# Performance work log

Hardware: AMD Instinct MI355X
Metric: run time of the kernel (lower is better)

Reference implementation:

```python
import jax, jax.numpy as jnp
import numpy as np

D_IN = 1024
D_OUT = 1024
N_HEADS = 16
D_H = D_OUT // N_HEADS


def setup_inputs() -> dict:
    key = jax.random.key(0)
    k_x, k_q, k_k, k_v = jax.random.split(key, 4)
    x = jax.random.normal(k_x, (4, 2048, D_IN), dtype=jnp.float32)
    s = 1.0 / np.sqrt(D_IN)
    # weights stored as [d_in, d_out] (transpose of torch Linear.weight)
    W_q = jax.random.uniform(k_q, (D_IN, D_OUT), dtype=jnp.float32, minval=-s, maxval=s)
    W_k = jax.random.uniform(k_k, (D_IN, D_OUT), dtype=jnp.float32, minval=-s, maxval=s)
    W_v = jax.random.uniform(k_v, (D_IN, D_OUT), dtype=jnp.float32, minval=-s, maxval=s)
    return {"x": x, "W_q": W_q, "W_k": W_k, "W_v": W_v}


def reference(x, W_q, W_k, W_v):
    B, T, _ = x.shape
    # QKV projections -> [B, H, T, d_h]
    def split_heads(y):
        return y.reshape(B, T, N_HEADS, D_H).transpose(0, 2, 1, 3)
    q = split_heads(x @ W_q)
    k = split_heads(x @ W_k)
    v = split_heads(x @ W_v)
    # attention scores [B, H, T, T]
    scores = jnp.einsum('bhqd,bhkd->bhqk', q, k)
    causal = jnp.tril(jnp.ones((T, T), dtype=bool))  # True = keep
    scores = jnp.where(causal, scores, -jnp.inf)
    weights = jax.nn.softmax(scores / np.sqrt(D_H), axis=-1)
    ctx = jnp.einsum('bhqk,bhkd->bhqd', weights, v)  # [B,H,T,d_h]
    return ctx.transpose(0, 2, 1, 3).reshape(B, T, D_OUT)
```

## Files before the change

### kernel.cpp

```cpp
#include <hip/hip_runtime.h>
#include <stdint.h>

typedef float f32x4 __attribute__((ext_vector_type(4)));
typedef __bf16 bf16x8 __attribute__((ext_vector_type(8)));

#define LOG2E 1.4426950408889634f
#define SCL2 (0.125f * LOG2E)

static __device__ __forceinline__ unsigned short f2bf(float f) {
  unsigned int u = __builtin_bit_cast(unsigned int, f);
  u += 0x7fffu + ((u >> 16) & 1u);
  return (unsigned short)(u >> 16);
}

static __device__ __forceinline__ void gload16(const void* g, void* l) {
  __builtin_amdgcn_global_load_lds(
      (const __attribute__((address_space(1))) unsigned int*)g,
      (__attribute__((address_space(3))) unsigned int*)l, 16, 0, 0);
}

__global__ void cvt_x_kernel(const float* __restrict__ x, unsigned short* __restrict__ xb) {
  size_t i = ((size_t)blockIdx.x * 256 + threadIdx.x) * 8;
  const float4 a = *(const float4*)(x + i);
  const float4 b = *(const float4*)(x + i + 4);
  union { unsigned short us[8]; uint4 u; } o;
  o.us[0] = f2bf(a.x); o.us[1] = f2bf(a.y); o.us[2] = f2bf(a.z); o.us[3] = f2bf(a.w);
  o.us[4] = f2bf(b.x); o.us[5] = f2bf(b.y); o.us[6] = f2bf(b.z); o.us[7] = f2bf(b.w);
  *(uint4*)(xb + i) = o.u;
}

__global__ void wt_kernel(const float* __restrict__ Wq, const float* __restrict__ Wk,
                          const float* __restrict__ Wv, unsigned short* __restrict__ Wt) {
  __shared__ float t[32][33];
  const int z = blockIdx.z;
  const float* W = (z == 0) ? Wq : ((z == 1) ? Wk : Wv);
  unsigned short* o = Wt + (size_t)z * 1048576;
  const int k0 = blockIdx.y * 32, n0 = blockIdx.x * 32;
  const int tx = threadIdx.x, ty = threadIdx.y;
#pragma unroll
  for (int i = 0; i < 4; ++i)
    t[ty + i * 8][tx] = W[(size_t)(k0 + ty + i * 8) * 1024 + n0 + tx];
  __syncthreads();
#pragma unroll
  for (int i = 0; i < 4; ++i)
    o[(size_t)(n0 + ty + i * 8) * 1024 + k0 + tx] = f2bf(t[tx][ty + i * 8]);
}

__global__ __launch_bounds__(256) void gemm_qkv(
    const unsigned short* __restrict__ xb, const unsigned short* __restrict__ Wt,
    unsigned short* __restrict__ Qb, unsigned short* __restrict__ Kb,
    unsigned short* __restrict__ Vtb) {
  __shared__ uint4 ldsab[2048];
  char* ldsc = (char*)ldsab;
  const int tid = threadIdx.x;
  const int lane = tid & 63;
  const int li = lane & 15, g = lane >> 4;
  const int wv = tid >> 6, wr = wv >> 1, wc = wv & 1;
  const int z = blockIdx.z;
  const int m0 = blockIdx.y * 128, n0 = blockIdx.x * 128;
  const char* Abase = (const char*)xb;
  const char* Bbase = (const char*)(Wt + (size_t)z * 1048576);

  const f32x4 fz = {0.f, 0.f, 0.f, 0.f};
  f32x4 acc[4][4];
#pragma unroll
  for (int m = 0; m < 4; ++m)
#pragma unroll
    for (int n = 0; n < 4; ++n) acc[m][n] = fz;

  for (int kt = 0; kt < 16; ++kt) {
    __syncthreads();
#pragma unroll
    for (int i = 0; i < 4; ++i) {
      const int c = i * 256 + tid, r = c >> 3, cr = c & 7;
      gload16(Abase + (size_t)(m0 + r) * 2048 + kt * 128 + ((cr ^ (r & 7)) * 16),
              ldsc + c * 16);
      gload16(Bbase + (size_t)(n0 + r) * 2048 + kt * 128 + ((cr ^ (r & 7)) * 16),
              ldsc + 16384 + c * 16);
    }
    __syncthreads();
#pragma unroll
    for (int ks = 0; ks < 2; ++ks) {
      bf16x8 a[4], b[4];
#pragma unroll
      for (int m = 0; m < 4; ++m) {
        const int ra = wr * 64 + m * 16 + li;
        a[m] = *(const bf16x8*)(ldsc + ra * 128 + (((ks * 4 + g) ^ (ra & 7)) * 16));
      }
#pragma unroll
      for (int n = 0; n < 4; ++n) {
        const int rb = wc * 64 + n * 16 + li;
        b[n] = *(const bf16x8*)(ldsc + 16384 + rb * 128 + (((ks * 4 + g) ^ (rb & 7)) * 16));
      }
#pragma unroll
      for (int m = 0; m < 4; ++m)
#pragma unroll
        for (int n = 0; n < 4; ++n)
          acc[m][n] = __builtin_amdgcn_mfma_f32_16x16x32_bf16(a[m], b[n], acc[m][n], 0, 0, 0);
    }
  }

  unsigned short* dst = (z == 0) ? Qb : ((z == 1) ? Kb : Vtb);
  const float sc = (z == 0) ? SCL2 : 1.0f;
#pragma unroll
  for (int m = 0; m < 4; ++m) {
#pragma unroll
    for (int r = 0; r < 4; ++r) {
      const int mg = m0 + wr * 64 + m * 16 + g * 4 + r;
      const int bI = mg >> 11, t = mg & 2047;
#pragma unroll
      for (int n = 0; n < 4; ++n) {
        const int ng = n0 + wc * 64 + n * 16 + li;
        const int h = ng >> 6, d = ng & 63;
        const unsigned short v = f2bf(acc[m][n][r] * sc);
        if (z == 2)
          dst[((size_t)(bI * 16 + h) * 64 + d) * 2048 + t] = v;
        else
          dst[((size_t)(bI * 16 + h) * 2048 + t) * 64 + d] = v;
      }
    }
  }
}

__global__ __launch_bounds__(512, 4) void attn_kernel(
    const unsigned short* __restrict__ Qb, const unsigned short* __restrict__ Kb,
    const unsigned short* __restrict__ Vtb, float* __restrict__ out) {
  __shared__ uint4 lds[4096];
  char* ldsc = (char*)lds;
  const int L = blockIdx.x;
  const int W = (L & 7) * 64 + (L >> 3);
  const int bh = W >> 3;
  const int qp = W & 7;
  const int tid = threadIdx.x;
  const int lane = tid & 63, wv = tid >> 6;
  const int grp = wv >> 2, wq = wv & 3;
  const int t256 = tid & 255;
  const int li = lane & 15, g = lane >> 4;

  char* gbase = ldsc + grp * 32768;

  const char* Qrow = (const char*)Qb + (size_t)bh * 2048 * 128;
  const char* Krow = (const char*)Kb + (size_t)bh * 2048 * 128;
  const char* Vrow = (const char*)Vtb + (size_t)bh * 64 * 4096;
  const int bI = bh >> 4, h = bh & 15;
  const f32x4 fz = {0.f, 0.f, 0.f, 0.f};

  union { unsigned int u[4]; bf16x8 v; } onesu;
  onesu.u[0] = 0x3F803F80u; onesu.u[1] = 0x3F803F80u;
  onesu.u[2] = 0x3F803F80u; onesu.u[3] = 0x3F803F80u;
  const bf16x8 ones = onesu.v;

  auto stage = [&](int b, int kt) {
#pragma unroll
    for (int i = 0; i < 2; ++i) {
      const int c = i * 256 + t256, r = c >> 3, cr = c & 7;
      gload16(Krow + (size_t)(kt * 64 + r) * 128 + ((cr ^ (r & 7)) * 16),
              gbase + b * 16384 + c * 16);
      gload16(Vrow + (size_t)r * 4096 + kt * 128 + ((cr ^ (r & 7)) * 16),
              gbase + b * 16384 + 8192 + c * 16);
    }
  };

  for (int half = 0; half < 2; ++half) {
    const int qt = half ? (15 - qp) : qp;
    const int q0 = qt * 128;
    const int qw = q0 + wq * 32;
    const int hc = qt + 1;
    const int kbeg = grp ? hc : 0;

    uint4 qf[2][2];
#pragma unroll
    for (int nq = 0; nq < 2; ++nq)
#pragma unroll
      for (int ks = 0; ks < 2; ++ks)
        qf[nq][ks] = *(const uint4*)(Qrow + (size_t)(qw + nq * 16 + li) * 128 + ks * 64 + g * 16);

    float mrow[2] = {-1e30f, -1e30f};
    float lrow[2] = {0.0f, 0.0f};
    f32x4 lsum[2] = {fz, fz};
    f32x4 ctx[4][2];
#pragma unroll
    for (int mtd = 0; mtd < 4; ++mtd)
#pragma unroll
      for (int nq = 0; nq < 2; ++nq) ctx[mtd][nq] = fz;

    stage(0, kbeg);

    for (int it = 0; it < hc; ++it) {
      const int kt = kbeg + it;
      __syncthreads();
      if (it + 1 < hc) stage((it + 1) & 1, kt + 1);
      if (kt * 64 > qw + 31) continue;

      const char* sK = gbase + (it & 1) * 16384;
      const char* sV = sK + 8192;

      f32x4 st[4][2];
#pragma unroll
      for (int mt = 0; mt < 4; ++mt)
#pragma unroll
        for (int nq = 0; nq < 2; ++nq) st[mt][nq] = fz;
      __builtin_amdgcn_s_setprio(1);
#pragma unroll
      for (int ks = 0; ks < 2; ++ks) {
        bf16x8 kf[4];
#pragma unroll
        for (int mt = 0; mt < 4; ++mt) {
          const int rk = mt * 16 + li;
          kf[mt] = *(const bf16x8*)(sK + rk * 128 + (((ks * 4 + g) ^ (rk & 7)) * 16));
        }
#pragma unroll
        for (int mt = 0; mt < 4; ++mt)
#pragma unroll
          for (int nq = 0; nq < 2; ++nq)
            st[mt][nq] = __builtin_amdgcn_mfma_f32_16x16x32_bf16(
                kf[mt], __builtin_bit_cast(bf16x8, qf[nq][ks]), st[mt][nq], 0, 0, 0);
      }
      __builtin_amdgcn_s_setprio(0);

      const bool full = (kt * 64 + 63 <= qw);
      bf16x8 pb[2][2];
#pragma unroll
      for (int nq = 0; nq < 2; ++nq) {
        float p[4][4];
        if (full) {
#pragma unroll
          for (int mt = 0; mt < 4; ++mt)
#pragma unroll
            for (int r = 0; r < 4; ++r) p[mt][r] = st[mt][nq][r];
        } else {
          const int qg_ = qw + nq * 16 + li;
#pragma unroll
          for (int mt = 0; mt < 4; ++mt)
#pragma unroll
            for (int r = 0; r < 4; ++r)
              p[mt][r] = (kt * 64 + mt * 16 + g * 4 + r > qg_) ? -__builtin_inff()
                                                               : st[mt][nq][r];
        }
        const float m1 = fmaxf(fmaxf(p[0][0], p[0][1]), p[0][2]);
        const float m2 = fmaxf(fmaxf(p[0][3], p[1][0]), p[1][1]);
        const float m3 = fmaxf(fmaxf(p[1][2], p[1][3]), p[2][0]);
        const float m4 = fmaxf(fmaxf(p[2][1], p[2][2]), p[2][3]);
        const float m5 = fmaxf(fmaxf(p[3][0], p[3][1]), p[3][2]);
        const float lmax = fmaxf(fmaxf(fmaxf(m1, m2), m3), fmaxf(fmaxf(m4, m5), p[3][3]));
        if (!__all(lmax <= mrow[nq] + 8.0f)) {
          float tmax = fmaxf(lmax, __shfl_xor(lmax, 16, 64));
          tmax = fmaxf(tmax, __shfl_xor(tmax, 32, 64));
          const float mnew = fmaxf(mrow[nq], tmax);
          const float resc = __builtin_amdgcn_exp2f(mrow[nq] - mnew);
          mrow[nq] = mnew;
          lsum[nq] = lsum[nq] * resc;
#pragma unroll
          for (int mtd = 0; mtd < 4; ++mtd) ctx[mtd][nq] = ctx[mtd][nq] * resc;
        }
        const float mcur = mrow[nq];
#pragma unroll
        for (int mt = 0; mt < 4; ++mt)
#pragma unroll
          for (int r = 0; r < 4; ++r)
            p[mt][r] = __builtin_amdgcn_exp2f(p[mt][r] - mcur);
#pragma unroll
        for (int ks2 = 0; ks2 < 2; ++ks2) {
          union { __bf16 b[8]; bf16x8 v; } u;
#pragma unroll
          for (int r = 0; r < 4; ++r) {
            u.b[r] = (__bf16)p[2 * ks2][r];
            u.b[4 + r] = (__bf16)p[2 * ks2 + 1][r];
          }
          pb[nq][ks2] = u.v;
        }
      }

      __builtin_amdgcn_s_setprio(1);
#pragma unroll
      for (int ks2 = 0; ks2 < 2; ++ks2) {
#pragma unroll
        for (int mtd = 0; mtd < 4; ++mtd) {
          const int rd = mtd * 16 + li;
          const char* vb = sV + rd * 128;
          const uint2 lo = *(const uint2*)(vb + (((ks2 * 4 + (g >> 1)) ^ (rd & 7)) * 16) + (g & 1) * 8);
          const uint2 hi = *(const uint2*)(vb + (((ks2 * 4 + 2 + (g >> 1)) ^ (rd & 7)) * 16) + (g & 1) * 8);
          uint4 vv; vv.x = lo.x; vv.y = lo.y; vv.z = hi.x; vv.w = hi.y;
          const bf16x8 vf = __builtin_bit_cast(bf16x8, vv);
#pragma unroll
          for (int nq = 0; nq < 2; ++nq)
            ctx[mtd][nq] = __builtin_amdgcn_mfma_f32_16x16x32_bf16(vf, pb[nq][ks2], ctx[mtd][nq], 0, 0, 0);
        }
#pragma unroll
        for (int nq = 0; nq < 2; ++nq)
          lsum[nq] = __builtin_amdgcn_mfma_f32_16x16x32_bf16(ones, pb[nq][ks2], lsum[nq], 0, 0, 0);
      }
      __builtin_amdgcn_s_setprio(0);
    }

    lrow[0] = lsum[0][0];
    lrow[1] = lsum[1][0];

    __syncthreads();
    if (grp == 1) {
      char* mb = ldsc + 32768;
#pragma unroll
      for (int nqp = 0; nqp < 2; ++nqp)
#pragma unroll
        for (int mtd = 0; mtd < 4; ++mtd)
          *(f32x4*)(mb + (wq * 64 + lane) * 128 + nqp * 64 + ((mtd ^ (lane & 3)) * 16)) = ctx[mtd][nqp];
      if (g == 0) {
#pragma unroll
        for (int nqp = 0; nqp < 2; ++nqp) {
          ((float*)ldsc)[nqp * 64 + wq * 16 + li] = mrow[nqp];
          ((float*)(ldsc + 512))[nqp * 64 + wq * 16 + li] = lrow[nqp];
        }
      }
    }
    __syncthreads();
    if (grp == 0) {
      const char* mb = ldsc + 32768;
#pragma unroll
      for (int nqp = 0; nqp < 2; ++nqp) {
        const float mB = ((const float*)ldsc)[nqp * 64 + wq * 16 + li];
        const float lB = ((const float*)(ldsc + 512))[nqp * 64 + wq * 16 + li];
        const float mM = fmaxf(mrow[nqp], mB);
        const float cA = __builtin_amdgcn_exp2f(mrow[nqp] - mM);
        const float cB = __builtin_amdgcn_exp2f(mB - mM);
        const float inv = 1.0f / (lrow[nqp] * cA + lB * cB);
        const float fA = cA * inv, fB = cB * inv;
#pragma unroll
        for (int mtd = 0; mtd < 4; ++mtd) {
          const f32x4 cb = *(const f32x4*)(mb + (wq * 64 + lane) * 128 + nqp * 64 + ((mtd ^ (lane & 3)) * 16));
          ctx[mtd][nqp] = ctx[mtd][nqp] * fA + cb * fB;
        }
      }
    }
    __syncthreads();

    if (grp == 0) {
      float* trb = (float*)(ldsc + wq * 8192);
#pragma unroll
      for (int nqp = 0; nqp < 2; ++nqp)
#pragma unroll
        for (int mtd = 0; mtd < 4; ++mtd)
#pragma unroll
          for (int r = 0; r < 4; ++r) {
            const int q = nqp * 16 + li;
            const int d = mtd * 16 + g * 4 + r;
            trb[q * 64 + ((((d >> 2) ^ (q & 15)) << 2) | (d & 3))] = ctx[mtd][nqp][r];
          }
    }
    __syncthreads();
    if (grp == 0) {
      const float* trb = (const float*)(ldsc + wq * 8192);
#pragma unroll
      for (int pass = 0; pass < 8; ++pass) {
        const int qr = pass * 4 + g;
        const float4 v = *(const float4*)&trb[qr * 64 + ((li ^ (qr & 15)) << 2)];
        *(float4*)(out + ((size_t)bI * 2048 + q0 + wq * 32 + qr) * 1024 + h * 64 + li * 4) = v;
      }
    }
    __syncthreads();
  }
}

extern "C" void kernel_launch(void* const* d_in, const int* in_sizes, int n_in,
                              void* d_out, int out_size, void* d_ws, size_t ws_size,
                              hipStream_t stream) {
  (void)in_sizes; (void)n_in; (void)out_size; (void)ws_size;
  const float* x  = (const float*)d_in[0];
  const float* Wq = (const float*)d_in[1];
  const float* Wk = (const float*)d_in[2];
  const float* Wv = (const float*)d_in[3];
  float* out = (float*)d_out;
  char* ws = (char*)d_ws;
  unsigned short* xb  = (unsigned short*)ws;
  unsigned short* Wt  = (unsigned short*)(ws + 16777216);
  unsigned short* Qb  = (unsigned short*)(ws + 23068672);
  unsigned short* Kb  = (unsigned short*)(ws + 39845888);
  unsigned short* Vtb = (unsigned short*)(ws + 56623104);

  hipLaunchKernelGGL(cvt_x_kernel, dim3(4096), dim3(256), 0, stream, x, xb);
  hipLaunchKernelGGL(wt_kernel, dim3(32, 32, 3), dim3(32, 8), 0, stream, Wq, Wk, Wv, Wt);
  hipLaunchKernelGGL(gemm_qkv, dim3(8, 64, 3), dim3(256), 0, stream, xb, Wt, Qb, Kb, Vtb);
  hipLaunchKernelGGL(attn_kernel, dim3(512), dim3(512), 0, stream, Qb, Kb, Vtb, out);
}
```

Before: 199.3 us.

## Stage V transpose through LDS and remap QKV GEMM blocks across XCDs

The V-projection epilogue previously wrote transposed bf16 values one 2-byte element at a time with a stride of 4 KB, so stores were badly uncoalesced. It now writes each wave's 64x64 tile into swizzled LDS and then emits 16-byte coalesced rows into Vt. The GEMM grid is also flattened to 1D with a remapping that spreads consecutive work across the 8 XCDs, which should improve L2 locality of shared A/B tiles. This adds an extra LDS round trip and a barrier in the V blocks.

```diff
diff --git a/kernel.cpp b/kernel.cpp
--- a/kernel.cpp
+++ b/kernel.cpp
@@ -56,8 +56,11 @@
   const int lane = tid & 63;
   const int li = lane & 15, g = lane >> 4;
   const int wv = tid >> 6, wr = wv >> 1, wc = wv & 1;
-  const int z = blockIdx.z;
-  const int m0 = blockIdx.y * 128, n0 = blockIdx.x * 128;
+  const int L = blockIdx.x;
+  const int W = (L & 7) * 192 + (L >> 3);
+  const int z = W >> 9;
+  const int rem = W & 511;
+  const int m0 = (rem >> 3) * 128, n0 = (rem & 7) * 128;
   const char* Abase = (const char*)xb;
   const char* Bbase = (const char*)(Wt + (size_t)z * 1048576);
 
@@ -100,23 +103,50 @@
     }
   }
 
-  unsigned short* dst = (z == 0) ? Qb : ((z == 1) ? Kb : Vtb);
-  const float sc = (z == 0) ? SCL2 : 1.0f;
-#pragma unroll
-  for (int m = 0; m < 4; ++m) {
-#pragma unroll
-    for (int r = 0; r < 4; ++r) {
-      const int mg = m0 + wr * 64 + m * 16 + g * 4 + r;
-      const int bI = mg >> 11, t = mg & 2047;
+  if (z == 2) {
+    __syncthreads();
+    char* tb = ldsc + wv * 8192;
+#pragma unroll
+    for (int m = 0; m < 4; ++m)
 #pragma unroll
       for (int n = 0; n < 4; ++n) {
-        const int ng = n0 + wc * 64 + n * 16 + li;
-        const int h = ng >> 6, d = ng & 63;
-        const unsigned short v = f2bf(acc[m][n][r] * sc);
-        if (z == 2)
-          dst[((size_t)(bI * 16 + h) * 64 + d) * 2048 + t] = v;
-        else
-          dst[((size_t)(bI * 16 + h) * 2048 + t) * 64 + d] = v;
+        const int d_l = n * 16 + li;
+#pragma unroll
+        for (int rp = 0; rp < 2; ++rp) {
+          const int t_l = m * 16 + g * 4 + rp * 2;
+          const unsigned lo = f2bf(acc[m][n][rp * 2]);
+          const unsigned hi2 = f2bf(acc[m][n][rp * 2 + 1]);
+          *(unsigned*)(tb + d_l * 128 + (((t_l >> 3) ^ (d_l & 7)) * 16) + (t_l & 7) * 2) =
+              lo | (hi2 << 16);
+        }
+      }
+    __syncthreads();
+    const int t0g = m0 + wr * 64;
+    const int bI2 = t0g >> 11, tt2 = t0g & 2047;
+    const int hh = (n0 + wc * 64) >> 6;
+#pragma unroll
+    for (int p2 = 0; p2 < 8; ++p2) {
+      const int d_l = p2 * 8 + (lane >> 3);
+      const int c8 = lane & 7;
+      const uint4 v = *(const uint4*)(tb + d_l * 128 + ((c8 ^ (d_l & 7)) * 16));
+      *(uint4*)((char*)Vtb +
+                ((((size_t)(bI2 * 16 + hh) * 64 + d_l) * 2048 + tt2 + c8 * 8) * 2)) = v;
+    }
+  } else {
+    unsigned short* dst = (z == 0) ? Qb : Kb;
+    const float sc = (z == 0) ? SCL2 : 1.0f;
+#pragma unroll
+    for (int m = 0; m < 4; ++m) {
+#pragma unroll
+      for (int r = 0; r < 4; ++r) {
+        const int mg = m0 + wr * 64 + m * 16 + g * 4 + r;
+        const int bI = mg >> 11, t = mg & 2047;
+#pragma unroll
+        for (int n = 0; n < 4; ++n) {
+          const int ng = n0 + wc * 64 + n * 16 + li;
+          const int h = ng >> 6, d = ng & 63;
+          dst[((size_t)(bI * 16 + h) * 2048 + t) * 64 + d] = f2bf(acc[m][n][r] * sc);
+        }
       }
     }
   }
@@ -378,6 +408,6 @@
 
   hipLaunchKernelGGL(cvt_x_kernel, dim3(4096), dim3(256), 0, stream, x, xb);
   hipLaunchKernelGGL(wt_kernel, dim3(32, 32, 3), dim3(32, 8), 0, stream, Wq, Wk, Wv, Wt);
-  hipLaunchKernelGGL(gemm_qkv, dim3(8, 64, 3), dim3(256), 0, stream, xb, Wt, Qb, Kb, Vtb);
+  hipLaunchKernelGGL(gemm_qkv, dim3(1536), dim3(256), 0, stream, xb, Wt, Qb, Kb, Vtb);
   hipLaunchKernelGGL(attn_kernel, dim3(512), dim3(512), 0, stream, Qb, Kb, Vtb, out);
 }
```

After: 178.5 us. 10.4% less time.
